# Kernel tuning notes

Measured on AMD Instinct MI355X. Metric: run time of the kernel, lower is better.

The kernel has to match this reference:

```python
import jax, jax.numpy as jnp
import numpy as np
import math

B, T, S, D, H = 2, 1024, 1024, 1024, 16
DH = D // H


def setup_inputs() -> dict:
    key = jax.random.key(0)
    ks = jax.random.split(key, 13)
    scale = 1.0 / math.sqrt(D)
    inp = {
        "q": jax.random.normal(ks[0], (B, T, D), jnp.float32),
        "k": jax.random.normal(ks[1], (B, S, D), jnp.float32),
        "v": jax.random.normal(ks[2], (B, S, D), jnp.float32),
        # causal mask: True means masked
        "attn_mask": jnp.broadcast_to(
            jnp.triu(jnp.ones((T, S), jnp.bool_), k=1)[None, None], (B, 1, T, S)
        ),
        "attn_bias": jax.random.normal(ks[3], (B, H, T, S), jnp.float32),
        "Wq": jax.random.normal(ks[4], (D, D), jnp.float32) * scale,
        "bq": jnp.zeros((D,), jnp.float32),
        "Wk": jax.random.normal(ks[5], (D, D), jnp.float32) * scale,
        "bk": jnp.zeros((D,), jnp.float32),
        "Wv": jax.random.normal(ks[6], (D, D), jnp.float32) * scale,
        "bv": jnp.zeros((D,), jnp.float32),
        "Wo": jax.random.normal(ks[7], (D, D), jnp.float32) * scale,
        "bo": jnp.zeros((D,), jnp.float32),
        "bias_scale": jnp.asarray(0.5, jnp.float32),
    }
    return inp


def reference(q, k, v, attn_mask, attn_bias, Wq, bq, Wk, bk, Wv, bv, Wo, bo, bias_scale):
    # projections (torch Linear convention: x @ W.T + b), split heads
    qh = (q @ Wq.T + bq).reshape(B, T, H, DH)   # (B,T,H,DH)
    kh = (k @ Wk.T + bk).reshape(B, S, H, DH)
    vh = (v @ Wv.T + bv).reshape(B, S, H, DH)

    scores = jnp.einsum("bthd,bshd->bhts", qh, kh) / math.sqrt(DH)  # (B,H,T,S)
    scores = jnp.clip(scores, -80.0, 80.0)
    scores = jnp.where(attn_mask, -jnp.inf, scores)  # mask broadcasts over H
    attn = jax.nn.softmax(scores, axis=-1)

    # post-softmax multiplicative bias + renormalize
    scale = 1.0 + bias_scale * jnp.tanh(attn_bias)
    attn = attn * jnp.maximum(scale, 1e-9)
    attn = attn / (jnp.sum(attn, axis=-1, keepdims=True) + 1e-9)

    # dropout p=0.0 (eval) -> identity
    out = jnp.einsum("bhts,bshd->bthd", attn, vh).reshape(B, T, D)
    out = out @ Wo.T + bo
    return out, attn
```

## Files before the change

### kernel.cpp

```cpp
#include <hip/hip_runtime.h>
#include <hip/hip_bf16.h>
#include <math.h>

#define BB 2
#define TT 1024
#define SS 1024
#define DD 1024
#define HH 16
#define DH 64

typedef __attribute__((ext_vector_type(8))) short bf16x8;
typedef __attribute__((ext_vector_type(4))) float f32x4;
typedef unsigned short ushort_t;

#define AS3(p) ((__attribute__((address_space(3))) unsigned int*)(p))
#define AS1(p) ((const __attribute__((address_space(1))) unsigned int*)(p))

__device__ __forceinline__ unsigned short f2b(float f) {
    union { float f; unsigned u; } x; x.f = f;
    unsigned r = x.u + 0x7FFFu + ((x.u >> 16) & 1u);
    return (unsigned short)(r >> 16);
}

__device__ __forceinline__ bf16x8 pack_bf16x8(float4 a, float4 b) {
    union { unsigned u[4]; bf16x8 v; } r;
    asm("v_cvt_pk_bf16_f32 %0, %1, %2" : "=v"(r.u[0]) : "v"(a.x), "v"(a.y));
    asm("v_cvt_pk_bf16_f32 %0, %1, %2" : "=v"(r.u[1]) : "v"(a.z), "v"(a.w));
    asm("v_cvt_pk_bf16_f32 %0, %1, %2" : "=v"(r.u[2]) : "v"(b.x), "v"(b.y));
    asm("v_cvt_pk_bf16_f32 %0, %1, %2" : "=v"(r.u[3]) : "v"(b.z), "v"(b.w));
    return r.v;
}

__global__ __launch_bounds__(256) void cvt3_kernel(
    const float* __restrict__ a, const float* __restrict__ b, const float* __restrict__ c,
    ushort_t* __restrict__ oa, ushort_t* __restrict__ ob, ushort_t* __restrict__ oc)
{
    const float* src = (blockIdx.y == 0) ? a : (blockIdx.y == 1) ? b : c;
    ushort_t* dst    = (blockIdx.y == 0) ? oa : (blockIdx.y == 1) ? ob : oc;
    size_t i = ((size_t)blockIdx.x * 256 + threadIdx.x) * 8;
    float4 v0 = *(const float4*)&src[i];
    float4 v1 = *(const float4*)&src[i + 4];
    uint4 o;
    o.x = f2b(v0.x) | ((unsigned)f2b(v0.y) << 16);
    o.y = f2b(v0.z) | ((unsigned)f2b(v0.w) << 16);
    o.z = f2b(v1.x) | ((unsigned)f2b(v1.y) << 16);
    o.w = f2b(v1.z) | ((unsigned)f2b(v1.w) << 16);
    *(uint4*)&dst[i] = o;
}

__global__ __launch_bounds__(256) void cvt4_kernel(
    const float* __restrict__ a, const float* __restrict__ b,
    const float* __restrict__ c, const float* __restrict__ d,
    ushort_t* __restrict__ oa, ushort_t* __restrict__ ob,
    ushort_t* __restrict__ oc, ushort_t* __restrict__ od)
{
    const float* src = (blockIdx.y == 0) ? a : (blockIdx.y == 1) ? b : (blockIdx.y == 2) ? c : d;
    ushort_t* dst    = (blockIdx.y == 0) ? oa : (blockIdx.y == 1) ? ob : (blockIdx.y == 2) ? oc : od;
    size_t i = ((size_t)blockIdx.x * 256 + threadIdx.x) * 8;
    float4 v0 = *(const float4*)&src[i];
    float4 v1 = *(const float4*)&src[i + 4];
    uint4 o;
    o.x = f2b(v0.x) | ((unsigned)f2b(v0.y) << 16);
    o.y = f2b(v0.z) | ((unsigned)f2b(v0.w) << 16);
    o.z = f2b(v1.x) | ((unsigned)f2b(v1.y) << 16);
    o.w = f2b(v1.z) | ((unsigned)f2b(v1.w) << 16);
    *(uint4*)&dst[i] = o;
}

__device__ __forceinline__ void gemm128_mainloop(
    const ushort_t* __restrict__ A,
    const ushort_t* __restrict__ Bw,
    int K, ushort_t* Asm, ushort_t* Bsm, f32x4 acc[4][4])
{
    const int tid = threadIdx.x;
    const int wave = tid >> 6, lane = tid & 63;
    const int sr8 = lane >> 3;
    const int gc8 = (lane & 7) ^ sr8;
    const int l15 = lane & 15, q = lane >> 4;
    const int mblk = (wave >> 1) * 64, nblk = (wave & 1) * 64;

    for (int k0 = 0; k0 < K; k0 += 64) {
        #pragma unroll
        for (int o = 0; o < 4; o++) {
            int r0 = wave * 32 + o * 8;
            __builtin_amdgcn_global_load_lds(AS1(A + (size_t)(r0 + sr8) * K + k0 + gc8 * 8),
                                             AS3(Asm + r0 * 64), 16, 0, 0);
            __builtin_amdgcn_global_load_lds(AS1(Bw + (size_t)(r0 + sr8) * K + k0 + gc8 * 8),
                                             AS3(Bsm + r0 * 64), 16, 0, 0);
        }
        __syncthreads();

        #pragma unroll
        for (int ks = 0; ks < 2; ks++) {
            bf16x8 av[4], bv[4];
            #pragma unroll
            for (int mi = 0; mi < 4; mi++) {
                int r = mblk + mi * 16 + l15;
                av[mi] = *(const bf16x8*)&Asm[r * 64 + ((ks * 4 + q) ^ (r & 7)) * 8];
            }
            #pragma unroll
            for (int ni = 0; ni < 4; ni++) {
                int r = nblk + ni * 16 + l15;
                bv[ni] = *(const bf16x8*)&Bsm[r * 64 + ((ks * 4 + q) ^ (r & 7)) * 8];
            }
            #pragma unroll
            for (int mi = 0; mi < 4; mi++)
                #pragma unroll
                for (int ni = 0; ni < 4; ni++)
                    acc[mi][ni] = __builtin_amdgcn_mfma_f32_16x16x32_bf16(av[mi], bv[ni], acc[mi][ni], 0, 0, 0);
        }
        __syncthreads();
    }
}

__global__ __launch_bounds__(256) void proj_gemm(
    const ushort_t* __restrict__ qb, const ushort_t* __restrict__ kb, const ushort_t* __restrict__ vb,
    const ushort_t* __restrict__ Wqb, const ushort_t* __restrict__ Wkb, const ushort_t* __restrict__ Wvb,
    const float* __restrict__ bq, const float* __restrict__ bk, const float* __restrict__ bv,
    ushort_t* __restrict__ qh, ushort_t* __restrict__ kh, ushort_t* __restrict__ vh)
{
    __shared__ ushort_t Asm[128 * 64];
    __shared__ ushort_t Bsm[128 * 64];
    const int z = blockIdx.z;
    const ushort_t* A = (z == 0) ? qb : (z == 1) ? kb : vb;
    const ushort_t* W = (z == 0) ? Wqb : (z == 1) ? Wkb : Wvb;
    const float* bias = (z == 0) ? bq : (z == 1) ? bk : bv;
    ushort_t* Y = (z == 0) ? qh : (z == 1) ? kh : vh;

    const int bm = blockIdx.y * 128, bn = blockIdx.x * 128;
    f32x4 acc[4][4];
    #pragma unroll
    for (int i = 0; i < 4; i++)
        #pragma unroll
        for (int j = 0; j < 4; j++) acc[i][j] = (f32x4)(0.f);

    gemm128_mainloop(A + (size_t)bm * DD, W + (size_t)bn * DD, DD, Asm, Bsm, acc);

    const int lane = threadIdx.x & 63, wave = threadIdx.x >> 6;
    const int mblk = (wave >> 1) * 64, nblk = (wave & 1) * 64;
    const int l15 = lane & 15, q = lane >> 4;
    #pragma unroll
    for (int mi = 0; mi < 4; mi++) {
        #pragma unroll
        for (int ni = 0; ni < 4; ni++) {
            int col = bn + nblk + ni * 16 + l15;
            float bcol = bias[col];
            #pragma unroll
            for (int r = 0; r < 4; r++) {
                int row = bm + mblk + mi * 16 + q * 4 + r;
                Y[(size_t)row * DD + col] = f2b(acc[mi][ni][r] + bcol);
            }
        }
    }
}

__global__ __launch_bounds__(256) void oproj_gemm(
    const ushort_t* __restrict__ A, const ushort_t* __restrict__ W,
    const float* __restrict__ bias, float* __restrict__ Y)
{
    __shared__ ushort_t Asm[128 * 64];
    __shared__ ushort_t Bsm[128 * 64];
    const int bm = blockIdx.y * 128, bn = blockIdx.x * 128;
    f32x4 acc[4][4];
    #pragma unroll
    for (int i = 0; i < 4; i++)
        #pragma unroll
        for (int j = 0; j < 4; j++) acc[i][j] = (f32x4)(0.f);

    gemm128_mainloop(A + (size_t)bm * DD, W + (size_t)bn * DD, DD, Asm, Bsm, acc);

    const int lane = threadIdx.x & 63, wave = threadIdx.x >> 6;
    const int mblk = (wave >> 1) * 64, nblk = (wave & 1) * 64;
    const int l15 = lane & 15, q = lane >> 4;
    #pragma unroll
    for (int mi = 0; mi < 4; mi++) {
        #pragma unroll
        for (int ni = 0; ni < 4; ni++) {
            int col = bn + nblk + ni * 16 + l15;
            float bcol = bias[col];
            #pragma unroll
            for (int r = 0; r < 4; r++) {
                int row = bm + mblk + mi * 16 + q * 4 + r;
                Y[(size_t)row * DD + col] = acc[mi][ni][r] + bcol;
            }
        }
    }
}

__global__ __launch_bounds__(256) void transpose_v(
    const ushort_t* __restrict__ vh, ushort_t* __restrict__ vT)
{
    __shared__ ushort_t Ls[64][72];
    const int s0 = blockIdx.x * 64;
    const int bh = blockIdx.y;
    const int b = bh >> 4, h = bh & 15;
    const int tid = threadIdx.x;
    const int r = tid >> 2, c16 = (tid & 3) * 16;

    const ushort_t* src = &vh[((size_t)(b * SS + s0 + r) * HH + h) * DH + c16];
    uint4 u0 = *(const uint4*)src;
    uint4 u1 = *(const uint4*)(src + 8);
    ushort_t tmp[16];
    *(uint4*)&tmp[0] = u0; *(uint4*)&tmp[8] = u1;
    #pragma unroll
    for (int j = 0; j < 16; j++) Ls[c16 + j][r] = tmp[j];
    __syncthreads();

    const int dh = r;
    uint4 w0 = *(const uint4*)&Ls[dh][c16];
    uint4 w1 = *(const uint4*)&Ls[dh][c16 + 8];
    ushort_t* dst = &vT[((size_t)bh * DH + dh) * SS + s0 + c16];
    *(uint4*)dst = w0;
    *(uint4*)(dst + 8) = w1;
}

__global__ __launch_bounds__(256) void scores_mfma(
    const ushort_t* __restrict__ qh, const ushort_t* __restrict__ kh,
    float* __restrict__ attn)
{
    __shared__ ushort_t Qs[128 * 64];
    __shared__ ushort_t Ks[128 * 64];

    int idx = blockIdx.x, ti = 0;
    while (idx >= ti + 1) { idx -= ti + 1; ti++; }
    const int si = idx;
    const int bh = blockIdx.y;
    const int b = bh >> 4, h = bh & 15;
    const int t0 = ti * 128, s0 = si * 128;

    const int tid = threadIdx.x;
    const int wave = tid >> 6, lane = tid & 63;
    const int sr8 = lane >> 3;
    const int gc8 = (lane & 7) ^ sr8;

    #pragma unroll
    for (int o = 0; o < 4; o++) {
        int r0 = (wave * 4 + o) * 8;
        int r = r0 + sr8;
        __builtin_amdgcn_global_load_lds(
            AS1(qh + ((size_t)(b * TT + t0 + r) * HH + h) * DH + gc8 * 8),
            AS3(Qs + r0 * 64), 16, 0, 0);
        __builtin_amdgcn_global_load_lds(
            AS1(kh + ((size_t)(b * SS + s0 + r) * HH + h) * DH + gc8 * 8),
            AS3(Ks + r0 * 64), 16, 0, 0);
    }
    __syncthreads();

    const int l15 = lane & 15, q = lane >> 4;
    const int tblk = (wave >> 1) * 64, sblk = (wave & 1) * 64;
    f32x4 acc[4][4];
    #pragma unroll
    for (int i = 0; i < 4; i++)
        #pragma unroll
        for (int j = 0; j < 4; j++) acc[i][j] = (f32x4)(0.f);

    #pragma unroll
    for (int ks = 0; ks < 2; ks++) {
        bf16x8 av[4], bv[4];
        #pragma unroll
        for (int mi = 0; mi < 4; mi++) {
            int r = tblk + mi * 16 + l15;
            av[mi] = *(const bf16x8*)&Qs[r * 64 + ((ks * 4 + q) ^ (r & 7)) * 8];
        }
        #pragma unroll
        for (int ni = 0; ni < 4; ni++) {
            int r = sblk + ni * 16 + l15;
            bv[ni] = *(const bf16x8*)&Ks[r * 64 + ((ks * 4 + q) ^ (r & 7)) * 8];
        }
        #pragma unroll
        for (int mi = 0; mi < 4; mi++)
            #pragma unroll
            for (int ni = 0; ni < 4; ni++)
                acc[mi][ni] = __builtin_amdgcn_mfma_f32_16x16x32_bf16(av[mi], bv[ni], acc[mi][ni], 0, 0, 0);
    }

    #pragma unroll
    for (int mi = 0; mi < 4; mi++) {
        #pragma unroll
        for (int ni = 0; ni < 4; ni++) {
            int scol = s0 + sblk + ni * 16 + l15;
            #pragma unroll
            for (int r = 0; r < 4; r++) {
                int t = t0 + tblk + mi * 16 + q * 4 + r;
                float v = acc[mi][ni][r] * 0.125f;
                v = fminf(fmaxf(v, -80.f), 80.f);
                attn[((size_t)bh * TT + t) * SS + scol] = v;
            }
        }
    }
}

__global__ __launch_bounds__(256) void softmax_bias_wave(
    const float* __restrict__ attn_bias, const float* __restrict__ bias_scale_p,
    float* __restrict__ attn)
{
    const int wave = threadIdx.x >> 6, lane = threadIdx.x & 63;
    const int row = blockIdx.x * 4 + wave;
    const int t = row & (TT - 1);

    float* prow = attn + (size_t)row * SS;
    const float* brow = attn_bias + (size_t)row * SS;
    const float bscale = bias_scale_p[0];

    const int nc = (t >> 8) + 1;

    float v[16];
    float m = -INFINITY;
    #pragma unroll
    for (int c = 0; c < 4; c++) {
        const int s0 = c * 256 + lane * 4;
        if (c < nc) {
            float4 rv = *(const float4*)&prow[s0];
            v[c * 4 + 0] = (s0     <= t) ? rv.x : -INFINITY;
            v[c * 4 + 1] = (s0 + 1 <= t) ? rv.y : -INFINITY;
            v[c * 4 + 2] = (s0 + 2 <= t) ? rv.z : -INFINITY;
            v[c * 4 + 3] = (s0 + 3 <= t) ? rv.w : -INFINITY;
            m = fmaxf(m, fmaxf(fmaxf(v[c*4], v[c*4+1]), fmaxf(v[c*4+2], v[c*4+3])));
        } else {
            v[c * 4 + 0] = -INFINITY; v[c * 4 + 1] = -INFINITY;
            v[c * 4 + 2] = -INFINITY; v[c * 4 + 3] = -INFINITY;
        }
    }
    #pragma unroll
    for (int off = 1; off < 64; off <<= 1)
        m = fmaxf(m, __shfl_xor(m, off));

    float w[16];
    float P = 0.f, Wn = 0.f;
    #pragma unroll
    for (int c = 0; c < 4; c++) {
        const int s0 = c * 256 + lane * 4;
        if (c < nc) {
            float4 bv = *(const float4*)&brow[s0];
            float bx[4] = {bv.x, bv.y, bv.z, bv.w};
            #pragma unroll
            for (int j = 0; j < 4; j++) {
                float vv = v[c * 4 + j];
                float p = (vv > -INFINITY) ? __expf(vv - m) : 0.f;
                float e = __expf(-2.f * fabsf(bx[j]));
                float th = copysignf((1.f - e) / (1.f + e), bx[j]);
                float sc = fmaxf(1.f + bscale * th, 1e-9f);
                float ww = p * sc;
                w[c * 4 + j] = ww;
                P += p; Wn += ww;
            }
        } else {
            w[c * 4 + 0] = 0.f; w[c * 4 + 1] = 0.f;
            w[c * 4 + 2] = 0.f; w[c * 4 + 3] = 0.f;
        }
    }
    #pragma unroll
    for (int off = 1; off < 64; off <<= 1) {
        P  += __shfl_xor(P, off);
        Wn += __shfl_xor(Wn, off);
    }
    const float inv = 1.f / (Wn + 1e-9f * P);

    #pragma unroll
    for (int c = 0; c < 4; c++) {
        const int s0 = c * 256 + lane * 4;
        float4 o;
        o.x = w[c * 4 + 0] * inv; o.y = w[c * 4 + 1] * inv;
        o.z = w[c * 4 + 2] * inv; o.w = w[c * 4 + 3] * inv;
        *(float4*)&prow[s0] = o;
    }
}

__global__ __launch_bounds__(256) void av_mfma(
    const float* __restrict__ attn, const ushort_t* __restrict__ vT,
    ushort_t* __restrict__ ao)
{
    __shared__ ushort_t Vsm[2][64 * 64];

    const int tb = (int)gridDim.x - 1 - (int)blockIdx.x;
    const int bh = blockIdx.y;
    const int b = bh >> 4, h = bh & 15;
    const int t0 = tb * 64;
    const int nsteps = tb + 1;

    const int tid = threadIdx.x;
    const int wave = tid >> 6, lane = tid & 63;
    const int sr8 = lane >> 3, gc8 = (lane & 7) ^ sr8;
    const int l15 = lane & 15, q = lane >> 4;

    const float* arow = attn + ((size_t)bh * TT + t0 + wave * 16 + l15) * SS + q * 8;
    const ushort_t* vbase = vT + (size_t)bh * DH * SS;

    f32x4 acc[4];
    #pragma unroll
    for (int i = 0; i < 4; i++) acc[i] = (f32x4)(0.f);

#define STAGE_V(sidx, buf) do {                                               \
        int s0_ = (sidx) * 64;                                                \
        _Pragma("unroll")                                                     \
        for (int o = 0; o < 2; o++) {                                         \
            int r0 = wave * 16 + o * 8;                                       \
            __builtin_amdgcn_global_load_lds(                                 \
                AS1(vbase + (size_t)(r0 + sr8) * SS + s0_ + gc8 * 8),         \
                AS3(&Vsm[buf][r0 * 64]), 16, 0, 0);                           \
        } } while (0)

#define LOAD_A(sidx, dst) do {                                                \
        const float* p_ = arow + (sidx) * 64;                                 \
        dst[0] = *(const float4*)(p_);                                        \
        dst[1] = *(const float4*)(p_ + 4);                                    \
        dst[2] = *(const float4*)(p_ + 32);                                   \
        dst[3] = *(const float4*)(p_ + 36); } while (0)

#define COMPUTE(buf, ax) do {                                                 \
        bf16x8 af0 = pack_bf16x8(ax[0], ax[1]);                               \
        bf16x8 af1 = pack_bf16x8(ax[2], ax[3]);                               \
        _Pragma("unroll")                                                     \
        for (int ni = 0; ni < 4; ni++) {                                      \
            int rv = ni * 16 + l15;                                           \
            bf16x8 b0 = *(const bf16x8*)&Vsm[buf][rv * 64 + ((q) ^ (rv & 7)) * 8];       \
            bf16x8 b1 = *(const bf16x8*)&Vsm[buf][rv * 64 + ((4 + q) ^ (rv & 7)) * 8];   \
            acc[ni] = __builtin_amdgcn_mfma_f32_16x16x32_bf16(af0, b0, acc[ni], 0, 0, 0);\
            acc[ni] = __builtin_amdgcn_mfma_f32_16x16x32_bf16(af1, b1, acc[ni], 0, 0, 0);\
        } } while (0)

    float4 aA[4], aB[4];
    STAGE_V(0, 0);
    LOAD_A(0, aA);
    __syncthreads();

    int st = 0;
    while (true) {
        if (st + 1 < nsteps) { STAGE_V(st + 1, 1); LOAD_A(st + 1, aB); }
        COMPUTE(0, aA);
        __syncthreads();
        if (++st == nsteps) break;
        if (st + 1 < nsteps) { STAGE_V(st + 1, 0); LOAD_A(st + 1, aA); }
        COMPUTE(1, aB);
        __syncthreads();
        if (++st == nsteps) break;
    }

#undef STAGE_V
#undef LOAD_A
#undef COMPUTE

    #pragma unroll
    for (int ni = 0; ni < 4; ni++) {
        int dh = ni * 16 + l15;
        #pragma unroll
        for (int r = 0; r < 4; r++) {
            int t = t0 + wave * 16 + q * 4 + r;
            ao[(size_t)(b * TT + t) * DD + h * DH + dh] = f2b(acc[ni][r]);
        }
    }
}

extern "C" void kernel_launch(void* const* d_in, const int* in_sizes, int n_in,
                              void* d_out, int out_size, void* d_ws, size_t ws_size,
                              hipStream_t stream)
{
    const float* q   = (const float*)d_in[0];
    const float* k   = (const float*)d_in[1];
    const float* v   = (const float*)d_in[2];
    const float* attn_bias = (const float*)d_in[4];
    const float* Wq = (const float*)d_in[5];
    const float* bq = (const float*)d_in[6];
    const float* Wk = (const float*)d_in[7];
    const float* bk = (const float*)d_in[8];
    const float* Wv = (const float*)d_in[9];
    const float* bv = (const float*)d_in[10];
    const float* Wo = (const float*)d_in[11];
    const float* bo = (const float*)d_in[12];
    const float* bscale = (const float*)d_in[13];

    char* base = (char*)d_ws;
    ushort_t* qb  = (ushort_t*)(base + (0ull << 20));
    ushort_t* kb  = (ushort_t*)(base + (4ull << 20));
    ushort_t* vb  = (ushort_t*)(base + (8ull << 20));
    ushort_t* Wqb = (ushort_t*)(base + (12ull << 20));
    ushort_t* Wkb = (ushort_t*)(base + (14ull << 20));
    ushort_t* Wvb = (ushort_t*)(base + (16ull << 20));
    ushort_t* Wob = (ushort_t*)(base + (18ull << 20));
    ushort_t* qhb = (ushort_t*)(base + (20ull << 20));
    ushort_t* khb = (ushort_t*)(base + (24ull << 20));
    ushort_t* vhb = (ushort_t*)(base + (28ull << 20));
    ushort_t* vT  = qb;
    ushort_t* aob = kb;

    float* out  = (float*)d_out;
    float* attn = out + (size_t)BB * TT * DD;

    cvt3_kernel<<<dim3(1024, 3), 256, 0, stream>>>(q, k, v, qb, kb, vb);
    cvt4_kernel<<<dim3(512, 4), 256, 0, stream>>>(Wq, Wk, Wv, Wo, Wqb, Wkb, Wvb, Wob);
    proj_gemm<<<dim3(8, 16, 3), 256, 0, stream>>>(qb, kb, vb, Wqb, Wkb, Wvb,
                                                  bq, bk, bv, qhb, khb, vhb);
    transpose_v<<<dim3(16, 32), 256, 0, stream>>>(vhb, vT);
    scores_mfma<<<dim3(36, 32), 256, 0, stream>>>(qhb, khb, attn);
    softmax_bias_wave<<<dim3(8192), 256, 0, stream>>>(attn_bias, bscale, attn);
    av_mfma<<<dim3(16, 32), 256, 0, stream>>>(attn, vT, aob);
    oproj_gemm<<<dim3(8, 16), 256, 0, stream>>>(aob, Wob, bo, out);
}
```

Before: 374.8 us.

## Double-buffer GEMM mainloop, merge conversion kernels, hoist bias loads in softmax

Result: faster. 367.4 us (-2.0%).

```diff
diff --git a/kernel.cpp b/kernel.cpp
--- a/kernel.cpp
+++ b/kernel.cpp
@@ -31,12 +31,22 @@
     return r.v;
 }
 
-__global__ __launch_bounds__(256) void cvt3_kernel(
-    const float* __restrict__ a, const float* __restrict__ b, const float* __restrict__ c,
-    ushort_t* __restrict__ oa, ushort_t* __restrict__ ob, ushort_t* __restrict__ oc)
-{
-    const float* src = (blockIdx.y == 0) ? a : (blockIdx.y == 1) ? b : c;
-    ushort_t* dst    = (blockIdx.y == 0) ? oa : (blockIdx.y == 1) ? ob : oc;
+__global__ __launch_bounds__(256) void cvt_all(
+    const float* __restrict__ q, const float* __restrict__ k, const float* __restrict__ v,
+    const float* __restrict__ Wq, const float* __restrict__ Wk,
+    const float* __restrict__ Wv, const float* __restrict__ Wo,
+    ushort_t* __restrict__ oq, ushort_t* __restrict__ ok, ushort_t* __restrict__ ov,
+    ushort_t* __restrict__ oWq, ushort_t* __restrict__ oWk,
+    ushort_t* __restrict__ oWv, ushort_t* __restrict__ oWo)
+{
+    const int y = blockIdx.y;
+    if (y >= 3 && blockIdx.x >= 512) return;
+    const float* src =
+        (y == 0) ? q : (y == 1) ? k : (y == 2) ? v :
+        (y == 3) ? Wq : (y == 4) ? Wk : (y == 5) ? Wv : Wo;
+    ushort_t* dst =
+        (y == 0) ? oq : (y == 1) ? ok : (y == 2) ? ov :
+        (y == 3) ? oWq : (y == 4) ? oWk : (y == 5) ? oWv : oWo;
     size_t i = ((size_t)blockIdx.x * 256 + threadIdx.x) * 8;
     float4 v0 = *(const float4*)&src[i];
     float4 v1 = *(const float4*)&src[i + 4];
@@ -48,69 +58,63 @@
     *(uint4*)&dst[i] = o;
 }
 
-__global__ __launch_bounds__(256) void cvt4_kernel(
-    const float* __restrict__ a, const float* __restrict__ b,
-    const float* __restrict__ c, const float* __restrict__ d,
-    ushort_t* __restrict__ oa, ushort_t* __restrict__ ob,
-    ushort_t* __restrict__ oc, ushort_t* __restrict__ od)
-{
-    const float* src = (blockIdx.y == 0) ? a : (blockIdx.y == 1) ? b : (blockIdx.y == 2) ? c : d;
-    ushort_t* dst    = (blockIdx.y == 0) ? oa : (blockIdx.y == 1) ? ob : (blockIdx.y == 2) ? oc : od;
-    size_t i = ((size_t)blockIdx.x * 256 + threadIdx.x) * 8;
-    float4 v0 = *(const float4*)&src[i];
-    float4 v1 = *(const float4*)&src[i + 4];
-    uint4 o;
-    o.x = f2b(v0.x) | ((unsigned)f2b(v0.y) << 16);
-    o.y = f2b(v0.z) | ((unsigned)f2b(v0.w) << 16);
-    o.z = f2b(v1.x) | ((unsigned)f2b(v1.y) << 16);
-    o.w = f2b(v1.z) | ((unsigned)f2b(v1.w) << 16);
-    *(uint4*)&dst[i] = o;
-}
-
 __device__ __forceinline__ void gemm128_mainloop(
     const ushort_t* __restrict__ A,
     const ushort_t* __restrict__ Bw,
-    int K, ushort_t* Asm, ushort_t* Bsm, f32x4 acc[4][4])
+    int K, ushort_t (*Asm)[128 * 32], ushort_t (*Bsm)[128 * 32],
+    f32x4 acc[4][4])
 {
     const int tid = threadIdx.x;
     const int wave = tid >> 6, lane = tid & 63;
-    const int sr8 = lane >> 3;
-    const int gc8 = (lane & 7) ^ sr8;
+    const int sr = lane >> 2;
+    const int gc = (lane & 3) ^ ((lane >> 3) & 3);
     const int l15 = lane & 15, q = lane >> 4;
     const int mblk = (wave >> 1) * 64, nblk = (wave & 1) * 64;
 
-    for (int k0 = 0; k0 < K; k0 += 64) {
-        #pragma unroll
-        for (int o = 0; o < 4; o++) {
-            int r0 = wave * 32 + o * 8;
-            __builtin_amdgcn_global_load_lds(AS1(A + (size_t)(r0 + sr8) * K + k0 + gc8 * 8),
-                                             AS3(Asm + r0 * 64), 16, 0, 0);
-            __builtin_amdgcn_global_load_lds(AS1(Bw + (size_t)(r0 + sr8) * K + k0 + gc8 * 8),
-                                             AS3(Bsm + r0 * 64), 16, 0, 0);
-        }
+#define G128_STAGE(k0_, b_) do {                                               \
+        _Pragma("unroll")                                                      \
+        for (int o = 0; o < 2; o++) {                                          \
+            int r0 = (wave * 2 + o) * 16;                                      \
+            __builtin_amdgcn_global_load_lds(                                  \
+                AS1(A + (size_t)(r0 + sr) * K + (k0_) + gc * 8),               \
+                AS3(Asm[b_] + r0 * 32), 16, 0, 0);                             \
+            __builtin_amdgcn_global_load_lds(                                  \
+                AS1(Bw + (size_t)(r0 + sr) * K + (k0_) + gc * 8),              \
+                AS3(Bsm[b_] + r0 * 32), 16, 0, 0);                             \
+        } } while (0)
+
+#define G128_COMPUTE(b_) do {                                                  \
+        bf16x8 av[4], bv[4];                                                   \
+        _Pragma("unroll")                                                      \
+        for (int mi = 0; mi < 4; mi++) {                                       \
+            int r = mblk + mi * 16 + l15;                                      \
+            av[mi] = *(const bf16x8*)&Asm[b_][r * 32 + (q ^ ((r >> 1) & 3)) * 8]; \
+        }                                                                      \
+        _Pragma("unroll")                                                      \
+        for (int ni = 0; ni < 4; ni++) {                                       \
+            int r = nblk + ni * 16 + l15;                                      \
+            bv[ni] = *(const bf16x8*)&Bsm[b_][r * 32 + (q ^ ((r >> 1) & 3)) * 8]; \
+        }                                                                      \
+        _Pragma("unroll")                                                      \
+        for (int mi = 0; mi < 4; mi++)                                         \
+            _Pragma("unroll")                                                  \
+            for (int ni = 0; ni < 4; ni++)                                     \
+                acc[mi][ni] = __builtin_amdgcn_mfma_f32_16x16x32_bf16(         \
+                    av[mi], bv[ni], acc[mi][ni], 0, 0, 0);                     \
+        } while (0)
+
+    G128_STAGE(0, 0);
+    __syncthreads();
+
+    int buf = 0;
+    for (int k0 = 0; k0 < K; k0 += 32) {
+        if (k0 + 32 < K) G128_STAGE(k0 + 32, buf ^ 1);
+        G128_COMPUTE(buf);
         __syncthreads();
-
-        #pragma unroll
-        for (int ks = 0; ks < 2; ks++) {
-            bf16x8 av[4], bv[4];
-            #pragma unroll
-            for (int mi = 0; mi < 4; mi++) {
-                int r = mblk + mi * 16 + l15;
-                av[mi] = *(const bf16x8*)&Asm[r * 64 + ((ks * 4 + q) ^ (r & 7)) * 8];
-            }
-            #pragma unroll
-            for (int ni = 0; ni < 4; ni++) {
-                int r = nblk + ni * 16 + l15;
-                bv[ni] = *(const bf16x8*)&Bsm[r * 64 + ((ks * 4 + q) ^ (r & 7)) * 8];
-            }
-            #pragma unroll
-            for (int mi = 0; mi < 4; mi++)
-                #pragma unroll
-                for (int ni = 0; ni < 4; ni++)
-                    acc[mi][ni] = __builtin_amdgcn_mfma_f32_16x16x32_bf16(av[mi], bv[ni], acc[mi][ni], 0, 0, 0);
-        }
-        __syncthreads();
-    }
+        buf ^= 1;
+    }
+#undef G128_STAGE
+#undef G128_COMPUTE
 }
 
 __global__ __launch_bounds__(256) void proj_gemm(
@@ -119,8 +123,8 @@
     const float* __restrict__ bq, const float* __restrict__ bk, const float* __restrict__ bv,
     ushort_t* __restrict__ qh, ushort_t* __restrict__ kh, ushort_t* __restrict__ vh)
 {
-    __shared__ ushort_t Asm[128 * 64];
-    __shared__ ushort_t Bsm[128 * 64];
+    __shared__ ushort_t Asm[2][128 * 32];
+    __shared__ ushort_t Bsm[2][128 * 32];
     const int z = blockIdx.z;
     const ushort_t* A = (z == 0) ? qb : (z == 1) ? kb : vb;
     const ushort_t* W = (z == 0) ? Wqb : (z == 1) ? Wkb : Wvb;
@@ -158,8 +162,8 @@
     const ushort_t* __restrict__ A, const ushort_t* __restrict__ W,
     const float* __restrict__ bias, float* __restrict__ Y)
 {
-    __shared__ ushort_t Asm[128 * 64];
-    __shared__ ushort_t Bsm[128 * 64];
+    __shared__ ushort_t Asm[2][128 * 32];
+    __shared__ ushort_t Bsm[2][128 * 32];
     const int bm = blockIdx.y * 128, bn = blockIdx.x * 128;
     f32x4 acc[4][4];
     #pragma unroll
@@ -305,12 +309,14 @@
     const int nc = (t >> 8) + 1;
 
     float v[16];
+    float4 bx[4];
     float m = -INFINITY;
     #pragma unroll
     for (int c = 0; c < 4; c++) {
         const int s0 = c * 256 + lane * 4;
         if (c < nc) {
             float4 rv = *(const float4*)&prow[s0];
+            bx[c] = *(const float4*)&brow[s0];
             v[c * 4 + 0] = (s0     <= t) ? rv.x : -INFINITY;
             v[c * 4 + 1] = (s0 + 1 <= t) ? rv.y : -INFINITY;
             v[c * 4 + 2] = (s0 + 2 <= t) ? rv.z : -INFINITY;
@@ -319,6 +325,7 @@
         } else {
             v[c * 4 + 0] = -INFINITY; v[c * 4 + 1] = -INFINITY;
             v[c * 4 + 2] = -INFINITY; v[c * 4 + 3] = -INFINITY;
+            bx[c] = make_float4(0.f, 0.f, 0.f, 0.f);
         }
     }
     #pragma unroll
@@ -329,16 +336,14 @@
     float P = 0.f, Wn = 0.f;
     #pragma unroll
     for (int c = 0; c < 4; c++) {
-        const int s0 = c * 256 + lane * 4;
         if (c < nc) {
-            float4 bv = *(const float4*)&brow[s0];
-            float bx[4] = {bv.x, bv.y, bv.z, bv.w};
+            float bxx[4] = {bx[c].x, bx[c].y, bx[c].z, bx[c].w};
             #pragma unroll
             for (int j = 0; j < 4; j++) {
                 float vv = v[c * 4 + j];
                 float p = (vv > -INFINITY) ? __expf(vv - m) : 0.f;
-                float e = __expf(-2.f * fabsf(bx[j]));
-                float th = copysignf((1.f - e) / (1.f + e), bx[j]);
+                float e = __expf(-2.f * fabsf(bxx[j]));
+                float th = copysignf((1.f - e) / (1.f + e), bxx[j]);
                 float sc = fmaxf(1.f + bscale * th, 1e-9f);
                 float ww = p * sc;
                 w[c * 4 + j] = ww;
@@ -486,8 +491,8 @@
     float* out  = (float*)d_out;
     float* attn = out + (size_t)BB * TT * DD;
 
-    cvt3_kernel<<<dim3(1024, 3), 256, 0, stream>>>(q, k, v, qb, kb, vb);
-    cvt4_kernel<<<dim3(512, 4), 256, 0, stream>>>(Wq, Wk, Wv, Wo, Wqb, Wkb, Wvb, Wob);
+    cvt_all<<<dim3(1024, 7), 256, 0, stream>>>(q, k, v, Wq, Wk, Wv, Wo,
+                                               qb, kb, vb, Wqb, Wkb, Wvb, Wob);
     proj_gemm<<<dim3(8, 16, 3), 256, 0, stream>>>(qb, kb, vb, Wqb, Wkb, Wvb,
                                                   bq, bk, bv, qhb, khb, vhb);
     transpose_v<<<dim3(16, 32), 256, 0, stream>>>(vhb, vT);
```
